# Performance work log

Measured on AMD Instinct MI355X. Metric: run time of the kernel, lower is better.

The kernel has to match this reference:

```python
import jax, jax.numpy as jnp
import numpy as np

B, A, D, F, BF = 256, 128, 8, 512, 16  # batch, max_atoms, max_degree, atom_feat, bond_feat


def setup_inputs() -> dict:
    key = jax.random.key(0)
    k1, k2, k3 = jax.random.split(key, 3)
    atoms = jax.random.normal(k1, (B, A, F), dtype=jnp.float32)
    bonds = jax.random.normal(k2, (B, A, D, BF), dtype=jnp.float32)
    # -1 is the padding value for missing neighbours (as in the original layer)
    edges = jax.random.randint(k3, (B, A, D), -1, A, dtype=jnp.int32)
    return {"atoms": atoms, "bonds": bonds, "edges": edges}


def reference(atoms, bonds, edges):
    # atoms: (B, A, F); edges: (B, A, D) with -1 padding; bonds unused by this layer
    b, a, f = atoms.shape
    # neighbour_lookup with maskvalue=-inf: prepend a -inf row so index 0 (= edge -1 + 1) maps to mask
    pad = jnp.full((b, 1, f), -jnp.inf, dtype=atoms.dtype)
    masked_atoms = jnp.concatenate([pad, atoms], axis=1)        # (B, A+1, F)
    masked_edges = edges + 1                                     # (B, A, D), in [0, A]
    neigh = masked_atoms[jnp.arange(b)[:, None, None], masked_edges]  # (B, A, D, F)
    # include_self=True: prepend each atom's own features
    all_feats = jnp.concatenate([atoms[:, :, None, :], neigh], axis=2)  # (B, A, D+1, F)
    max_features = jnp.max(all_feats, axis=2)                   # (B, A, F)
    atom_degrees = jnp.sum(edges != -1, axis=-1, keepdims=True)  # (B, A, 1)
    general_atom_mask = (atom_degrees != 0).astype(atoms.dtype)
    return max_features * general_atom_mask
```

## Files before the change

### kernel.cpp

```cpp
#include <hip/hip_runtime.h>

#define B_ 256
#define A_ 128
#define D_ 8
#define F_ 512
#define FC 32
#define NCHUNK (F_ / FC)
#define THREADS 256
#define NXCD 8

typedef float vfloat4 __attribute__((ext_vector_type(4)));

typedef __attribute__((address_space(3))) void        as3_void;
typedef const __attribute__((address_space(1))) void  as1_void;

__device__ __forceinline__ void gload_lds16(const void* g, void* l) {
    __builtin_amdgcn_global_load_lds((as1_void*)g, (as3_void*)l, 16, 0, 0);
}

__global__ __launch_bounds__(THREADS) void NeuralGraphPool_kernel(
    const float* __restrict__ atoms,
    const int*   __restrict__ edges,
    float*       __restrict__ out)
{
    __shared__ float slab[A_ * FC];
    __shared__ int   eds[A_ * D_];

    const int hw  = blockIdx.x;
    const int blk = (hw & (NXCD - 1)) * ((B_ * NCHUNK) / NXCD) + (hw >> 3);

    const int b   = blk >> 4;
    const int fc0 = (blk & (NCHUNK - 1)) * FC;
    const int t   = threadIdx.x;

    const float* __restrict__ abase = atoms + (size_t)b * (A_ * F_) + fc0;

    gload_lds16(edges + (size_t)b * (A_ * D_) + t * 4, eds + t * 4);

#pragma unroll
    for (int j = 0; j < (A_ * FC / 4) / THREADS; ++j) {
        const int fi = j * THREADS + t;
        const int a  = fi >> 3;
        const int c  = fi & 7;
        gload_lds16(abase + a * F_ + c * 4, slab + fi * 4);
    }
    __syncthreads();

#pragma unroll
    for (int k = 0; k < (A_ * FC / 4) / THREADS; ++k) {
        const int o = k * THREADS + t;
        const int a = o >> 3;
        const int c = (o & 7) * 4;

        int e[D_];
        int degree = 0;
#pragma unroll
        for (int d = 0; d < D_; ++d) {
            e[d] = eds[a * D_ + d];
            degree += (e[d] >= 0) ? 1 : 0;
        }

        vfloat4 acc = *reinterpret_cast<const vfloat4*>(slab + a * FC + c);
#pragma unroll
        for (int d = 0; d < D_; ++d) {
            const int row = (e[d] >= 0) ? e[d] : a;
            const vfloat4 v = *reinterpret_cast<const vfloat4*>(slab + row * FC + c);
            acc.x = fmaxf(acc.x, v.x);
            acc.y = fmaxf(acc.y, v.y);
            acc.z = fmaxf(acc.z, v.z);
            acc.w = fmaxf(acc.w, v.w);
        }

        vfloat4 r = acc;
        if (degree == 0) r = (vfloat4)(0.f);
        *reinterpret_cast<vfloat4*>(
            out + (size_t)b * (A_ * F_) + a * F_ + fc0 + c) = r;
    }
}

extern "C" void kernel_launch(void* const* d_in, const int* in_sizes, int n_in,
                              void* d_out, int out_size, void* d_ws, size_t ws_size,
                              hipStream_t stream) {
    const float* atoms = (const float*)d_in[0];
    const int*   edges = (const int*)d_in[2];
    float*       out   = (float*)d_out;

    dim3 grid(B_ * NCHUNK);
    dim3 block(THREADS);
    hipLaunchKernelGGL(NeuralGraphPool_kernel, grid, block, 0, stream,
                       atoms, edges, out);
}
```

Baseline: 25.28 us.

## Process two feature chunks per block with overlapped second-chunk loading

Each block now covers two adjacent 32-wide feature chunks instead of one, which halves the grid. It issues LDS-direct loads for both slabs up front, waits only for the edges and the first slab via a partial vmcnt, and computes the first chunk while the second slab is still arriving. The edge list is loaded once per pair of chunks. The cost is double the LDS per block, a hand-counted vmcnt that must match the number of issued loads, and fewer blocks available to hide latency.

Result: no change. 25.76 us (+1.9%).

```diff
diff --git a/kernel.cpp b/kernel.cpp
--- a/kernel.cpp
+++ b/kernel.cpp
@@ -5,9 +5,11 @@
 #define D_ 8
 #define F_ 512
 #define FC 32
-#define NCHUNK (F_ / FC)
+#define CPB 2
+#define NPAIR (F_ / (FC*CPB))
 #define THREADS 256
 #define NXCD 8
+#define NBLK (B_ * NPAIR)
 
 typedef float vfloat4 __attribute__((ext_vector_type(4)));
 
@@ -18,34 +20,12 @@
     __builtin_amdgcn_global_load_lds((as1_void*)g, (as3_void*)l, 16, 0, 0);
 }
 
-__global__ __launch_bounds__(THREADS) void NeuralGraphPool_kernel(
-    const float* __restrict__ atoms,
-    const int*   __restrict__ edges,
-    float*       __restrict__ out)
+__device__ __forceinline__ void compute_chunk(
+    const float* __restrict__ slab,
+    const int*   __restrict__ eds,
+    float*       __restrict__ obase,
+    int t)
 {
-    __shared__ float slab[A_ * FC];
-    __shared__ int   eds[A_ * D_];
-
-    const int hw  = blockIdx.x;
-    const int blk = (hw & (NXCD - 1)) * ((B_ * NCHUNK) / NXCD) + (hw >> 3);
-
-    const int b   = blk >> 4;
-    const int fc0 = (blk & (NCHUNK - 1)) * FC;
-    const int t   = threadIdx.x;
-
-    const float* __restrict__ abase = atoms + (size_t)b * (A_ * F_) + fc0;
-
-    gload_lds16(edges + (size_t)b * (A_ * D_) + t * 4, eds + t * 4);
-
-#pragma unroll
-    for (int j = 0; j < (A_ * FC / 4) / THREADS; ++j) {
-        const int fi = j * THREADS + t;
-        const int a  = fi >> 3;
-        const int c  = fi & 7;
-        gload_lds16(abase + a * F_ + c * 4, slab + fi * 4);
-    }
-    __syncthreads();
-
 #pragma unroll
     for (int k = 0; k < (A_ * FC / 4) / THREADS; ++k) {
         const int o = k * THREADS + t;
@@ -73,9 +53,53 @@
 
         vfloat4 r = acc;
         if (degree == 0) r = (vfloat4)(0.f);
-        *reinterpret_cast<vfloat4*>(
-            out + (size_t)b * (A_ * F_) + a * F_ + fc0 + c) = r;
+        *reinterpret_cast<vfloat4*>(obase + a * F_ + c) = r;
     }
+}
+
+__global__ __launch_bounds__(THREADS) void NeuralGraphPool_kernel(
+    const float* __restrict__ atoms,
+    const int*   __restrict__ edges,
+    float*       __restrict__ out)
+{
+    __shared__ float slab[CPB][A_ * FC];
+    __shared__ int   eds[A_ * D_];
+
+    const int hw = blockIdx.x;
+    const int p  = (hw & (NXCD - 1)) * (NBLK / NXCD) + (hw >> 3);
+
+    const int b   = p >> 3;
+    const int fc0 = (p & (NPAIR - 1)) * (FC * CPB);
+    const int t   = threadIdx.x;
+
+    const float* __restrict__ abase = atoms + (size_t)b * (A_ * F_) + fc0;
+    float*       __restrict__ obase = out   + (size_t)b * (A_ * F_) + fc0;
+
+    gload_lds16(edges + (size_t)b * (A_ * D_) + t * 4, eds + t * 4);
+#pragma unroll
+    for (int j = 0; j < (A_ * FC / 4) / THREADS; ++j) {
+        const int fi = j * THREADS + t;
+        const int a  = fi >> 3;
+        const int c  = fi & 7;
+        gload_lds16(abase + a * F_ + c * 4, &slab[0][fi * 4]);
+    }
+#pragma unroll
+    for (int j = 0; j < (A_ * FC / 4) / THREADS; ++j) {
+        const int fi = j * THREADS + t;
+        const int a  = fi >> 3;
+        const int c  = fi & 7;
+        gload_lds16(abase + FC + a * F_ + c * 4, &slab[1][fi * 4]);
+    }
+
+    asm volatile("s_waitcnt vmcnt(4)" ::: "memory");
+    __builtin_amdgcn_s_barrier();
+    __builtin_amdgcn_sched_barrier(0);
+
+    compute_chunk(slab[0], eds, obase, t);
+
+    __syncthreads();
+
+    compute_chunk(slab[1], eds, obase + FC, t);
 }
 
 extern "C" void kernel_launch(void* const* d_in, const int* in_sizes, int n_in,
@@ -85,7 +109,7 @@
     const int*   edges = (const int*)d_in[2];
     float*       out   = (float*)d_out;
 
-    dim3 grid(B_ * NCHUNK);
+    dim3 grid(NBLK);
     dim3 block(THREADS);
     hipLaunchKernelGGL(NeuralGraphPool_kernel, grid, block, 0, stream,
                        atoms, edges, out);
```
